# Performance work log

Measured on AMD Instinct MI355X. Metric: run time of the kernel, lower is better.

The kernel has to match this reference:

```python
import jax, jax.numpy as jnp
import numpy as np

NUM_NODES = 50000


def setup_inputs() -> dict:
    key = jax.random.key(0)
    ks = jax.random.split(key, 5)
    d = 128
    E = 600000
    x = jax.random.normal(ks[0], (NUM_NODES, d), dtype=jnp.float32)
    edge_attr = jax.random.normal(ks[1], (E, d), dtype=jnp.float32)
    receivers_idx = jax.random.randint(ks[2], (E,), 0, NUM_NODES)
    # MLP params: Linear(2d -> d), ReLU, Linear(d -> d). Stored as [in, out].
    W1 = jax.random.normal(ks[3], (2 * d, d), dtype=jnp.float32) / np.sqrt(2 * d)
    b1 = jnp.zeros((d,), dtype=jnp.float32)
    W2 = jax.random.normal(ks[4], (d, d), dtype=jnp.float32) / np.sqrt(d)
    b2 = jnp.zeros((d,), dtype=jnp.float32)
    return {"x": x, "edge_attr": edge_attr, "receivers_idx": receivers_idx,
            "W1": W1, "b1": b1, "W2": W2, "b2": b2}


def reference(x, edge_attr, receivers_idx, W1, b1, W2, b2):
    # scatter_add(edge_attr, receivers_idx, dim=0, dim_size=num_nodes)
    agg = jax.ops.segment_sum(edge_attr, receivers_idx, num_segments=NUM_NODES)  # [N, d]
    collected = jnp.concatenate([x, agg], axis=-1)  # [N, 2d]
    h = jax.nn.relu(collected @ W1 + b1)  # [N, d]
    out = h @ W2 + b2                     # [N, d]
    # Original returns Data(x=out, edge_attr=edge_attr, edge_index=edge_index);
    # edge_attr/edge_index pass through unchanged, so return the new node features.
    return out
```

## Files before the change

### kernel.cpp

```cpp
#include <hip/hip_runtime.h>
#include <hip/hip_bf16.h>

#define N_NODES 50000
#define DIM 128
#define N_EDGES 600000
#define MAX_DEG 64

typedef __attribute__((ext_vector_type(8))) short short8;
typedef __attribute__((ext_vector_type(4))) float f32x4;

__device__ __forceinline__ unsigned short f2bf_u(float f) {
    return __bfloat16_as_ushort(__float2bfloat16(f));
}

#define FILL_BLOCKS ((N_EDGES + 255) / 256)
#define PREP_BLOCKS 192

__global__ __launch_bounds__(256) void fill_prep(
    const int* __restrict__ ridx, int* __restrict__ cnt, int* __restrict__ elist,
    const float* __restrict__ W1, const float* __restrict__ W2,
    __hip_bfloat16* __restrict__ W1t, __hip_bfloat16* __restrict__ W2t) {
    int b = blockIdx.x;
    if (b < FILL_BLOCKS) {
        int e = b * 256 + threadIdx.x;
        if (e < N_EDGES) {
            int node = ridx[e];
            int pos = atomicAdd(&cnt[node], 1);
            if (pos < MAX_DEG) elist[(size_t)node * MAX_DEG + pos] = e;
        }
    } else {
        int t = (b - FILL_BLOCKS) * 256 + threadIdx.x;
        if (t < 256 * 128) {
            int k = t >> 7, n = t & 127;
            W1t[n * 256 + k] = __float2bfloat16(W1[t]);
        } else {
            int q = t - 256 * 128;
            int k = q >> 7, n = q & 127;
            W2t[n * 128 + k] = __float2bfloat16(W2[q]);
        }
    }
}

__global__ __launch_bounds__(256) void aggregate_kernel(
    const float* __restrict__ edge_attr,
    const int* __restrict__ elist,
    const int* __restrict__ cnt,
    __hip_bfloat16* __restrict__ agg) {
    const int node = blockIdx.x * 4 + (threadIdx.x >> 6);
    const int lane = threadIdx.x & 63;
    if (node >= N_NODES) return;
    int deg = cnt[node];
    deg = deg < MAX_DEG ? deg : MAX_DEG;
    const int* el = elist + (size_t)node * MAX_DEG;
    float sx = 0.f, sy = 0.f;
    int j = 0;
    for (; j + 8 <= deg; j += 8) {
        int4 ea = *reinterpret_cast<const int4*>(el + j);
        int4 eb = *reinterpret_cast<const int4*>(el + j + 4);
        float2 v0 = *reinterpret_cast<const float2*>(edge_attr + (size_t)ea.x * DIM + lane * 2);
        float2 v1 = *reinterpret_cast<const float2*>(edge_attr + (size_t)ea.y * DIM + lane * 2);
        float2 v2 = *reinterpret_cast<const float2*>(edge_attr + (size_t)ea.z * DIM + lane * 2);
        float2 v3 = *reinterpret_cast<const float2*>(edge_attr + (size_t)ea.w * DIM + lane * 2);
        float2 v4 = *reinterpret_cast<const float2*>(edge_attr + (size_t)eb.x * DIM + lane * 2);
        float2 v5 = *reinterpret_cast<const float2*>(edge_attr + (size_t)eb.y * DIM + lane * 2);
        float2 v6 = *reinterpret_cast<const float2*>(edge_attr + (size_t)eb.z * DIM + lane * 2);
        float2 v7 = *reinterpret_cast<const float2*>(edge_attr + (size_t)eb.w * DIM + lane * 2);
        sx += ((v0.x + v1.x) + (v2.x + v3.x)) + ((v4.x + v5.x) + (v6.x + v7.x));
        sy += ((v0.y + v1.y) + (v2.y + v3.y)) + ((v4.y + v5.y) + (v6.y + v7.y));
    }
    if (j + 4 <= deg) {
        int4 ea = *reinterpret_cast<const int4*>(el + j);
        float2 v0 = *reinterpret_cast<const float2*>(edge_attr + (size_t)ea.x * DIM + lane * 2);
        float2 v1 = *reinterpret_cast<const float2*>(edge_attr + (size_t)ea.y * DIM + lane * 2);
        float2 v2 = *reinterpret_cast<const float2*>(edge_attr + (size_t)ea.z * DIM + lane * 2);
        float2 v3 = *reinterpret_cast<const float2*>(edge_attr + (size_t)ea.w * DIM + lane * 2);
        sx += (v0.x + v1.x) + (v2.x + v3.x);
        sy += (v0.y + v1.y) + (v2.y + v3.y);
        j += 4;
    }
    for (; j < deg; j++) {
        int e0 = el[j];
        float2 v0 = *reinterpret_cast<const float2*>(edge_attr + (size_t)e0 * DIM + lane * 2);
        sx += v0.x;
        sy += v0.y;
    }
    unsigned packed = ((unsigned)f2bf_u(sy) << 16) | (unsigned)f2bf_u(sx);
    *reinterpret_cast<unsigned*>(agg + (size_t)node * DIM + lane * 2) = packed;
}

__global__ __launch_bounds__(256) void mlp_kernel(
    const float* __restrict__ x,
    const __hip_bfloat16* __restrict__ agg,
    const __hip_bfloat16* __restrict__ W1t,
    const float* __restrict__ b1,
    const __hip_bfloat16* __restrict__ W2t,
    const float* __restrict__ b2,
    float* __restrict__ out) {
    __shared__ __hip_bfloat16 sH[64][136];

    const int wave = threadIdx.x >> 6;
    const int lane = threadIdx.x & 63;
    const int quad = lane >> 4;
    const int l16  = lane & 15;
    const int rowBase = blockIdx.x * 64 + wave * 16;

    int rowA = rowBase + l16;
    rowA = rowA < N_NODES ? rowA : N_NODES - 1;

    f32x4 accH[8] = {};
#pragma unroll
    for (int ks = 0; ks < 8; ks++) {
        const int k0 = ks * 32 + quad * 8;
        short8 a;
        if (ks < 4) {
            const float* xp = x + (size_t)rowA * DIM + k0;
            f32x4 u = *reinterpret_cast<const f32x4*>(xp);
            f32x4 v = *reinterpret_cast<const f32x4*>(xp + 4);
            short8 av = { (short)f2bf_u(u[0]), (short)f2bf_u(u[1]),
                          (short)f2bf_u(u[2]), (short)f2bf_u(u[3]),
                          (short)f2bf_u(v[0]), (short)f2bf_u(v[1]),
                          (short)f2bf_u(v[2]), (short)f2bf_u(v[3]) };
            a = av;
        } else {
            a = *reinterpret_cast<const short8*>(agg + (size_t)rowA * DIM + (k0 - 128));
        }
#pragma unroll
        for (int nt = 0; nt < 8; nt++) {
            short8 b = *reinterpret_cast<const short8*>(W1t + (nt * 16 + l16) * 256 + k0);
            accH[nt] = __builtin_amdgcn_mfma_f32_16x16x32_bf16(a, b, accH[nt], 0, 0, 0);
        }
    }

#pragma unroll
    for (int nt = 0; nt < 8; nt++) {
        const float bias = b1[nt * 16 + l16];
#pragma unroll
        for (int i = 0; i < 4; i++) {
            float v = accH[nt][i] + bias;
            v = v > 0.0f ? v : 0.0f;
            int r = wave * 16 + quad * 4 + i;
            sH[r][nt * 16 + l16] = __float2bfloat16(v);
        }
    }

    f32x4 accO[8] = {};
#pragma unroll
    for (int ks = 0; ks < 4; ks++) {
        const int k0 = ks * 32 + quad * 8;
        short8 a = *reinterpret_cast<const short8*>(&sH[wave * 16 + l16][k0]);
#pragma unroll
        for (int nt = 0; nt < 8; nt++) {
            short8 b = *reinterpret_cast<const short8*>(W2t + (nt * 16 + l16) * 128 + k0);
            accO[nt] = __builtin_amdgcn_mfma_f32_16x16x32_bf16(a, b, accO[nt], 0, 0, 0);
        }
    }

#pragma unroll
    for (int nt = 0; nt < 8; nt++) {
        const float bias = b2[nt * 16 + l16];
#pragma unroll
        for (int i = 0; i < 4; i++) {
            int row = rowBase + quad * 4 + i;
            if (row < N_NODES) {
                out[(size_t)row * DIM + nt * 16 + l16] = accO[nt][i] + bias;
            }
        }
    }
}

extern "C" void kernel_launch(void* const* d_in, const int* in_sizes, int n_in,
                              void* d_out, int out_size, void* d_ws, size_t ws_size,
                              hipStream_t stream) {
    const float* x         = (const float*)d_in[0];
    const float* edge_attr = (const float*)d_in[1];
    const int*   ridx      = (const int*)d_in[2];
    const float* W1        = (const float*)d_in[3];
    const float* b1        = (const float*)d_in[4];
    const float* W2        = (const float*)d_in[5];
    const float* b2        = (const float*)d_in[6];
    float* out = (float*)d_out;

    char* w = (char*)d_ws;
    int* elist = (int*)w;                     w += (size_t)N_NODES * MAX_DEG * 4;
    int* cnt   = (int*)w;                     w += (size_t)N_NODES * 4;
    __hip_bfloat16* agg = (__hip_bfloat16*)w; w += (size_t)N_NODES * DIM * 2;
    __hip_bfloat16* W1t = (__hip_bfloat16*)w; w += 256 * 128 * 2;
    __hip_bfloat16* W2t = (__hip_bfloat16*)w;

    hipMemsetAsync(cnt, 0, (size_t)N_NODES * 4, stream);
    fill_prep<<<dim3(FILL_BLOCKS + PREP_BLOCKS), dim3(256), 0, stream>>>(
        ridx, cnt, elist, W1, W2, W1t, W2t);
    aggregate_kernel<<<dim3((N_NODES + 3) / 4), dim3(256), 0, stream>>>(
        edge_attr, elist, cnt, agg);
    mlp_kernel<<<dim3((N_NODES + 63) / 64), dim3(256), 0, stream>>>(
        x, agg, W1t, b1, W2t, b2, out);
}
```

Baseline: 531.5 us.

## Fuse edge aggregation into the MLP kernel via a shared-memory input tile

```diff
diff --git a/kernel.cpp b/kernel.cpp
--- a/kernel.cpp
+++ b/kernel.cpp
@@ -41,128 +41,121 @@
     }
 }
 
-__global__ __launch_bounds__(256) void aggregate_kernel(
+__global__ __launch_bounds__(512) void gather_mlp(
+    const float* __restrict__ x,
     const float* __restrict__ edge_attr,
     const int* __restrict__ elist,
     const int* __restrict__ cnt,
-    __hip_bfloat16* __restrict__ agg) {
-    const int node = blockIdx.x * 4 + (threadIdx.x >> 6);
-    const int lane = threadIdx.x & 63;
-    if (node >= N_NODES) return;
-    int deg = cnt[node];
-    deg = deg < MAX_DEG ? deg : MAX_DEG;
-    const int* el = elist + (size_t)node * MAX_DEG;
-    float sx = 0.f, sy = 0.f;
-    int j = 0;
-    for (; j + 8 <= deg; j += 8) {
-        int4 ea = *reinterpret_cast<const int4*>(el + j);
-        int4 eb = *reinterpret_cast<const int4*>(el + j + 4);
-        float2 v0 = *reinterpret_cast<const float2*>(edge_attr + (size_t)ea.x * DIM + lane * 2);
-        float2 v1 = *reinterpret_cast<const float2*>(edge_attr + (size_t)ea.y * DIM + lane * 2);
-        float2 v2 = *reinterpret_cast<const float2*>(edge_attr + (size_t)ea.z * DIM + lane * 2);
-        float2 v3 = *reinterpret_cast<const float2*>(edge_attr + (size_t)ea.w * DIM + lane * 2);
-        float2 v4 = *reinterpret_cast<const float2*>(edge_attr + (size_t)eb.x * DIM + lane * 2);
-        float2 v5 = *reinterpret_cast<const float2*>(edge_attr + (size_t)eb.y * DIM + lane * 2);
-        float2 v6 = *reinterpret_cast<const float2*>(edge_attr + (size_t)eb.z * DIM + lane * 2);
-        float2 v7 = *reinterpret_cast<const float2*>(edge_attr + (size_t)eb.w * DIM + lane * 2);
-        sx += ((v0.x + v1.x) + (v2.x + v3.x)) + ((v4.x + v5.x) + (v6.x + v7.x));
-        sy += ((v0.y + v1.y) + (v2.y + v3.y)) + ((v4.y + v5.y) + (v6.y + v7.y));
-    }
-    if (j + 4 <= deg) {
-        int4 ea = *reinterpret_cast<const int4*>(el + j);
-        float2 v0 = *reinterpret_cast<const float2*>(edge_attr + (size_t)ea.x * DIM + lane * 2);
-        float2 v1 = *reinterpret_cast<const float2*>(edge_attr + (size_t)ea.y * DIM + lane * 2);
-        float2 v2 = *reinterpret_cast<const float2*>(edge_attr + (size_t)ea.z * DIM + lane * 2);
-        float2 v3 = *reinterpret_cast<const float2*>(edge_attr + (size_t)ea.w * DIM + lane * 2);
-        sx += (v0.x + v1.x) + (v2.x + v3.x);
-        sy += (v0.y + v1.y) + (v2.y + v3.y);
-        j += 4;
-    }
-    for (; j < deg; j++) {
-        int e0 = el[j];
-        float2 v0 = *reinterpret_cast<const float2*>(edge_attr + (size_t)e0 * DIM + lane * 2);
-        sx += v0.x;
-        sy += v0.y;
-    }
-    unsigned packed = ((unsigned)f2bf_u(sy) << 16) | (unsigned)f2bf_u(sx);
-    *reinterpret_cast<unsigned*>(agg + (size_t)node * DIM + lane * 2) = packed;
-}
-
-__global__ __launch_bounds__(256) void mlp_kernel(
-    const float* __restrict__ x,
-    const __hip_bfloat16* __restrict__ agg,
     const __hip_bfloat16* __restrict__ W1t,
     const float* __restrict__ b1,
     const __hip_bfloat16* __restrict__ W2t,
     const float* __restrict__ b2,
     float* __restrict__ out) {
-    __shared__ __hip_bfloat16 sH[64][136];
+    __shared__ __hip_bfloat16 sIn[32][264];
+    __shared__ __hip_bfloat16 sH[32][136];
 
     const int wave = threadIdx.x >> 6;
     const int lane = threadIdx.x & 63;
     const int quad = lane >> 4;
     const int l16  = lane & 15;
-    const int rowBase = blockIdx.x * 64 + wave * 16;
+    const int rowBase = blockIdx.x * 32;
 
-    int rowA = rowBase + l16;
-    rowA = rowA < N_NODES ? rowA : N_NODES - 1;
+    for (int i = 0; i < 4; i++) {
+        const int r = wave * 4 + i;
+        const int node = rowBase + r;
+        unsigned px = 0u, pa = 0u;
+        if (node < N_NODES) {
+            float2 xv = *reinterpret_cast<const float2*>(x + (size_t)node * DIM + lane * 2);
+            px = ((unsigned)f2bf_u(xv.y) << 16) | (unsigned)f2bf_u(xv.x);
+            int deg = cnt[node];
+            deg = deg < MAX_DEG ? deg : MAX_DEG;
+            const int* el = elist + (size_t)node * MAX_DEG;
+            float sx = 0.f, sy = 0.f;
+            int j = 0;
+            for (; j + 8 <= deg; j += 8) {
+                int4 ea = *reinterpret_cast<const int4*>(el + j);
+                int4 eb = *reinterpret_cast<const int4*>(el + j + 4);
+                float2 v0 = *reinterpret_cast<const float2*>(edge_attr + (size_t)ea.x * DIM + lane * 2);
+                float2 v1 = *reinterpret_cast<const float2*>(edge_attr + (size_t)ea.y * DIM + lane * 2);
+                float2 v2 = *reinterpret_cast<const float2*>(edge_attr + (size_t)ea.z * DIM + lane * 2);
+                float2 v3 = *reinterpret_cast<const float2*>(edge_attr + (size_t)ea.w * DIM + lane * 2);
+                float2 v4 = *reinterpret_cast<const float2*>(edge_attr + (size_t)eb.x * DIM + lane * 2);
+                float2 v5 = *reinterpret_cast<const float2*>(edge_attr + (size_t)eb.y * DIM + lane * 2);
+                float2 v6 = *reinterpret_cast<const float2*>(edge_attr + (size_t)eb.z * DIM + lane * 2);
+                float2 v7 = *reinterpret_cast<const float2*>(edge_attr + (size_t)eb.w * DIM + lane * 2);
+                sx += ((v0.x + v1.x) + (v2.x + v3.x)) + ((v4.x + v5.x) + (v6.x + v7.x));
+                sy += ((v0.y + v1.y) + (v2.y + v3.y)) + ((v4.y + v5.y) + (v6.y + v7.y));
+            }
+            if (j + 4 <= deg) {
+                int4 ea = *reinterpret_cast<const int4*>(el + j);
+                float2 v0 = *reinterpret_cast<const float2*>(edge_attr + (size_t)ea.x * DIM + lane * 2);
+                float2 v1 = *reinterpret_cast<const float2*>(edge_attr + (size_t)ea.y * DIM + lane * 2);
+                float2 v2 = *reinterpret_cast<const float2*>(edge_attr + (size_t)ea.z * DIM + lane * 2);
+                float2 v3 = *reinterpret_cast<const float2*>(edge_attr + (size_t)ea.w * DIM + lane * 2);
+                sx += (v0.x + v1.x) + (v2.x + v3.x);
+                sy += (v0.y + v1.y) + (v2.y + v3.y);
+                j += 4;
+            }
+            for (; j < deg; j++) {
+                int e0 = el[j];
+                float2 v0 = *reinterpret_cast<const float2*>(edge_attr + (size_t)e0 * DIM + lane * 2);
+                sx += v0.x;
+                sy += v0.y;
+            }
+            pa = ((unsigned)f2bf_u(sy) << 16) | (unsigned)f2bf_u(sx);
+        }
+        *reinterpret_cast<unsigned*>(&sIn[r][lane * 2]) = px;
+        *reinterpret_cast<unsigned*>(&sIn[r][128 + lane * 2]) = pa;
+    }
+    __syncthreads();
 
-    f32x4 accH[8] = {};
+    const int wm = wave >> 2;
+    const int colBase = (wave & 3) * 32;
+
+    f32x4 accH[2] = {};
 #pragma unroll
     for (int ks = 0; ks < 8; ks++) {
         const int k0 = ks * 32 + quad * 8;
-        short8 a;
-        if (ks < 4) {
-            const float* xp = x + (size_t)rowA * DIM + k0;
-            f32x4 u = *reinterpret_cast<const f32x4*>(xp);
-            f32x4 v = *reinterpret_cast<const f32x4*>(xp + 4);
-            short8 av = { (short)f2bf_u(u[0]), (short)f2bf_u(u[1]),
-                          (short)f2bf_u(u[2]), (short)f2bf_u(u[3]),
-                          (short)f2bf_u(v[0]), (short)f2bf_u(v[1]),
-                          (short)f2bf_u(v[2]), (short)f2bf_u(v[3]) };
-            a = av;
-        } else {
-            a = *reinterpret_cast<const short8*>(agg + (size_t)rowA * DIM + (k0 - 128));
-        }
+        short8 a = *reinterpret_cast<const short8*>(&sIn[wm * 16 + l16][k0]);
 #pragma unroll
-        for (int nt = 0; nt < 8; nt++) {
-            short8 b = *reinterpret_cast<const short8*>(W1t + (nt * 16 + l16) * 256 + k0);
+        for (int nt = 0; nt < 2; nt++) {
+            short8 b = *reinterpret_cast<const short8*>(W1t + (colBase + nt * 16 + l16) * 256 + k0);
             accH[nt] = __builtin_amdgcn_mfma_f32_16x16x32_bf16(a, b, accH[nt], 0, 0, 0);
         }
     }
 
 #pragma unroll
-    for (int nt = 0; nt < 8; nt++) {
-        const float bias = b1[nt * 16 + l16];
+    for (int nt = 0; nt < 2; nt++) {
+        const float bias = b1[colBase + nt * 16 + l16];
 #pragma unroll
         for (int i = 0; i < 4; i++) {
             float v = accH[nt][i] + bias;
             v = v > 0.0f ? v : 0.0f;
-            int r = wave * 16 + quad * 4 + i;
-            sH[r][nt * 16 + l16] = __float2bfloat16(v);
+            sH[wm * 16 + quad * 4 + i][colBase + nt * 16 + l16] = __float2bfloat16(v);
         }
     }
+    __syncthreads();
 
-    f32x4 accO[8] = {};
+    f32x4 accO[2] = {};
 #pragma unroll
     for (int ks = 0; ks < 4; ks++) {
         const int k0 = ks * 32 + quad * 8;
-        short8 a = *reinterpret_cast<const short8*>(&sH[wave * 16 + l16][k0]);
+        short8 a = *reinterpret_cast<const short8*>(&sH[wm * 16 + l16][k0]);
 #pragma unroll
-        for (int nt = 0; nt < 8; nt++) {
-            short8 b = *reinterpret_cast<const short8*>(W2t + (nt * 16 + l16) * 128 + k0);
+        for (int nt = 0; nt < 2; nt++) {
+            short8 b = *reinterpret_cast<const short8*>(W2t + (colBase + nt * 16 + l16) * 128 + k0);
             accO[nt] = __builtin_amdgcn_mfma_f32_16x16x32_bf16(a, b, accO[nt], 0, 0, 0);
         }
     }
 
 #pragma unroll
-    for (int nt = 0; nt < 8; nt++) {
-        const float bias = b2[nt * 16 + l16];
+    for (int nt = 0; nt < 2; nt++) {
+        const float bias = b2[colBase + nt * 16 + l16];
 #pragma unroll
         for (int i = 0; i < 4; i++) {
-            int row = rowBase + quad * 4 + i;
+            int row = rowBase + wm * 16 + quad * 4 + i;
             if (row < N_NODES) {
-                out[(size_t)row * DIM + nt * 16 + l16] = accO[nt][i] + bias;
+                out[(size_t)row * DIM + colBase + nt * 16 + l16] = accO[nt][i] + bias;
             }
         }
     }
@@ -183,15 +176,12 @@
     char* w = (char*)d_ws;
     int* elist = (int*)w;                     w += (size_t)N_NODES * MAX_DEG * 4;
     int* cnt   = (int*)w;                     w += (size_t)N_NODES * 4;
-    __hip_bfloat16* agg = (__hip_bfloat16*)w; w += (size_t)N_NODES * DIM * 2;
     __hip_bfloat16* W1t = (__hip_bfloat16*)w; w += 256 * 128 * 2;
     __hip_bfloat16* W2t = (__hip_bfloat16*)w;
 
     hipMemsetAsync(cnt, 0, (size_t)N_NODES * 4, stream);
     fill_prep<<<dim3(FILL_BLOCKS + PREP_BLOCKS), dim3(256), 0, stream>>>(
         ridx, cnt, elist, W1, W2, W1t, W2t);
-    aggregate_kernel<<<dim3((N_NODES + 3) / 4), dim3(256), 0, stream>>>(
-        edge_attr, elist, cnt, agg);
-    mlp_kernel<<<dim3((N_NODES + 63) / 64), dim3(256), 0, stream>>>(
-        x, agg, W1t, b1, W2t, b2, out);
+    gather_mlp<<<dim3((N_NODES + 31) / 32), dim3(512), 0, stream>>>(
+        x, edge_attr, elist, cnt, W1t, b1, W2t, b2, out);
 }
```

New measurement: 519.3 us. 2.3% less time.
